# Optimization experiments

Hardware: AMD Instinct MI355X
Metric: run time of the kernel (lower is better)

## Reference

```python
import jax, jax.numpy as jnp
import numpy as np

N, E, D = 50000, 600000, 128
LN_EPS = 1e-5


def setup_inputs() -> dict:
    key = jax.random.key(0)
    ks = jax.random.split(key, 7)
    s = 1.0 / np.sqrt(D)
    x = jax.random.normal(ks[0], (N, D), dtype=jnp.float32)
    edge_index = jax.random.randint(ks[1], (2, E), 0, N, dtype=jnp.int32)
    Wq = jax.random.normal(ks[2], (D, D), dtype=jnp.float32) * s
    Wk = jax.random.normal(ks[3], (D, D), dtype=jnp.float32) * s
    Wv = jax.random.normal(ks[4], (D, D), dtype=jnp.float32) * s
    Wo = jax.random.normal(ks[5], (D, D), dtype=jnp.float32) * s
    bo = jnp.zeros((D,), dtype=jnp.float32)
    gamma = jnp.ones((D,), dtype=jnp.float32)
    beta = jnp.zeros((D,), dtype=jnp.float32)
    return {"x": x, "edge_index": edge_index, "Wq": Wq, "Wk": Wk,
            "Wv": Wv, "Wo": Wo, "bo": bo, "gamma": gamma, "beta": beta}


def reference(x, edge_index, Wq, Wk, Wv, Wo, bo, gamma, beta):
    src, dst = edge_index[0], edge_index[1]
    # gather endpoint features, project (torch Linear: y = x @ W.T)
    q = x[dst] @ Wq.T                      # [E, D]
    k = x[src] @ Wk.T                      # [E, D]
    v = x[src] @ Wv.T                      # [E, D]
    logits = jnp.sum(q * k, axis=-1, keepdims=True) / np.sqrt(D)  # [E, 1]
    msg = jax.nn.sigmoid(logits) * v       # [E, D]
    agg = jax.ops.segment_sum(msg, dst, num_segments=N)  # scatter-add -> [N, D]
    out = agg @ Wo.T + bo
    h = x + out
    # LayerNorm over last dim
    mu = jnp.mean(h, axis=-1, keepdims=True)
    var = jnp.mean(jnp.square(h - mu), axis=-1, keepdims=True)
    return (h - mu) * jax.lax.rsqrt(var + LN_EPS) * gamma + beta
```

## Files before the change

### kernel.cpp

```cpp
#include <hip/hip_runtime.h>
#include <math.h>


#define BM 64
#define QSCALE -0.08838834764831845f

typedef __attribute__((ext_vector_type(8))) short bfrag;
typedef __attribute__((ext_vector_type(4))) float f32x4;

__device__ __forceinline__ short f2bf(float f) {
    union { float f; unsigned u; } v; v.f = f;
    unsigned r = v.u + 0x7FFFu + ((v.u >> 16) & 1u);
    return (short)(r >> 16);
}
__device__ __forceinline__ float bf2f(short h) {
    union { unsigned u; float f; } v;
    v.u = ((unsigned)(unsigned short)h) << 16;
    return v.f;
}
__device__ __forceinline__ float klo(unsigned w) {
    union { unsigned u; float f; } v; v.u = w << 16; return v.f;
}
__device__ __forceinline__ float vhi(unsigned w) {
    union { unsigned u; float f; } v; v.u = w & 0xffff0000u; return v.f;
}

#define SWZ(x, pat) __int_as_float(__builtin_amdgcn_ds_swizzle(__float_as_int(x), pat))

__global__ __launch_bounds__(256) void zero_prep(
    const float* __restrict__ Wq, const float* __restrict__ Wk,
    const float* __restrict__ Wv, const float* __restrict__ Wo,
    short* __restrict__ whi, short* __restrict__ wlo,
    int* __restrict__ hist, int N)
{
    int g = blockIdx.x * 256 + threadIdx.x;
    if (g < N) hist[g] = 0;
    if (g < 65536) {
        const float* Ws[4] = {Wq, Wk, Wv, Wo};
        float f = Ws[g >> 14][g & 16383];
        short h = f2bf(f);
        short l = f2bf(f - bf2f(h));
        whi[g] = h; wlo[g] = l;
    }
}

__global__ __launch_bounds__(256) void qkv_mfma(
    const float* __restrict__ x,
    const short* __restrict__ whi, const short* __restrict__ wlo,
    unsigned short* __restrict__ Q16, unsigned short* __restrict__ KV16, int N)
{
    __shared__ short xs_hi[64][136];
    __shared__ short xs_lo[64][136];

    const int tid = threadIdx.x;
    const int row0 = blockIdx.x * BM;
    const int mat  = blockIdx.y;

    #pragma unroll
    for (int i = 0; i < 8; ++i) {
        int idx = tid + 256 * i;
        int r = idx >> 5;
        int c4 = idx & 31;
        int gr = row0 + r;
        float4 val = make_float4(0.f, 0.f, 0.f, 0.f);
        if (gr < N) val = ((const float4*)(x + (size_t)gr * 128))[c4];
        short4 h, l;
        h.x = f2bf(val.x); l.x = f2bf(val.x - bf2f(h.x));
        h.y = f2bf(val.y); l.y = f2bf(val.y - bf2f(h.y));
        h.z = f2bf(val.z); l.z = f2bf(val.z - bf2f(h.z));
        h.w = f2bf(val.w); l.w = f2bf(val.w - bf2f(h.w));
        *((short4*)&xs_hi[r][c4 * 4]) = h;
        *((short4*)&xs_lo[r][c4 * 4]) = l;
    }
    __syncthreads();

    const int wid  = tid >> 6;
    const int lane = tid & 63;
    const int n16  = lane & 15;
    const int quad = lane >> 4;

    const short* __restrict__ WH = whi + mat * 16384;
    const short* __restrict__ WL = wlo + mat * 16384;
    const f32x4 zero = {0.f, 0.f, 0.f, 0.f};
    f32x4 acc[4][2];
    #pragma unroll
    for (int t = 0; t < 4; ++t) { acc[t][0] = zero; acc[t][1] = zero; }

    #pragma unroll
    for (int kc = 0; kc < 4; ++kc) {
        int k0 = kc * 32 + quad * 8;
        bfrag ah[4], al[4], bh[2], bl[2];
        #pragma unroll
        for (int t = 0; t < 4; ++t) {
            ah[t] = *((const bfrag*)&xs_hi[t * 16 + n16][k0]);
            al[t] = *((const bfrag*)&xs_lo[t * 16 + n16][k0]);
        }
        #pragma unroll
        for (int c = 0; c < 2; ++c) {
            int wr = (wid * 2 + c) * 16 + n16;
            bh[c] = *((const bfrag*)(WH + wr * 128 + k0));
            bl[c] = *((const bfrag*)(WL + wr * 128 + k0));
        }
        #pragma unroll
        for (int t = 0; t < 4; ++t)
            #pragma unroll
            for (int c = 0; c < 2; ++c) {
                acc[t][c] = __builtin_amdgcn_mfma_f32_16x16x32_bf16(ah[t], bh[c], acc[t][c], 0, 0, 0);
                acc[t][c] = __builtin_amdgcn_mfma_f32_16x16x32_bf16(al[t], bh[c], acc[t][c], 0, 0, 0);
                acc[t][c] = __builtin_amdgcn_mfma_f32_16x16x32_bf16(ah[t], bl[c], acc[t][c], 0, 0, 0);
            }
    }

    #pragma unroll
    for (int t = 0; t < 4; ++t)
        #pragma unroll
        for (int r = 0; r < 4; ++r) {
            int grow = row0 + t * 16 + quad * 4 + r;
            if (grow < N) {
                int c0 = (wid * 2 + 0) * 16 + n16;
                int c1 = (wid * 2 + 1) * 16 + n16;
                if (mat == 0) {
                    Q16[(size_t)grow * 128 + c0] = (unsigned short)f2bf(acc[t][0][r] * QSCALE);
                    Q16[(size_t)grow * 128 + c1] = (unsigned short)f2bf(acc[t][1][r] * QSCALE);
                } else {
                    size_t base = (size_t)grow * 256 + (mat - 1);
                    KV16[base + 2 * c0] = (unsigned short)f2bf(acc[t][0][r]);
                    KV16[base + 2 * c1] = (unsigned short)f2bf(acc[t][1][r]);
                }
            }
        }
}

__global__ __launch_bounds__(256) void hist_kernel(
    const int* __restrict__ ei, int* __restrict__ hist, int E)
{
    int e = blockIdx.x * blockDim.x + threadIdx.x;
    if (e < E) atomicAdd(&hist[ei[E + e]], 1);
}

#define SCAN_TPB 256
#define SCAN_EPT 4

__global__ __launch_bounds__(SCAN_TPB) void scan_partial(
    const int* __restrict__ hist, int* __restrict__ offs,
    int* __restrict__ blockSums, int N)
{
    __shared__ int sdata[SCAN_TPB];
    int b = blockIdx.x;
    int t = threadIdx.x;
    int base = b * SCAN_TPB * SCAN_EPT + t * SCAN_EPT;
    int v[SCAN_EPT];
    int tot = 0;
    #pragma unroll
    for (int j = 0; j < SCAN_EPT; ++j) {
        int idx = base + j;
        v[j] = (idx < N) ? hist[idx] : 0;
        tot += v[j];
    }
    sdata[t] = tot;
    __syncthreads();
    for (int off = 1; off < SCAN_TPB; off <<= 1) {
        int xv = (t >= off) ? sdata[t - off] : 0;
        __syncthreads();
        sdata[t] += xv;
        __syncthreads();
    }
    int run = sdata[t] - tot;
    #pragma unroll
    for (int j = 0; j < SCAN_EPT; ++j) {
        int idx = base + j;
        if (idx < N) offs[idx] = run;
        run += v[j];
    }
    if (t == SCAN_TPB - 1) blockSums[b] = sdata[t];
}

__global__ __launch_bounds__(256) void scan_add(
    int* __restrict__ offs, int* __restrict__ starts,
    const int* __restrict__ blockSums, int N, int nb)
{
    __shared__ int bs[64];
    int t = threadIdx.x;
    if (t < 64) {
        int v = (t < nb) ? blockSums[t] : 0;
        #pragma unroll
        for (int off = 1; off < 64; off <<= 1) {
            int u = __shfl_up(v, off);
            if (t >= off) v += u;
        }
        bs[t] = v;
    }
    __syncthreads();
    int idx = blockIdx.x * blockDim.x + threadIdx.x;
    if (idx < N) {
        int blk = idx >> 10;
        int pref = (blk == 0) ? 0 : bs[blk - 1];
        int vv = offs[idx] + pref;
        offs[idx] = vv;
        starts[idx] = vv;
    }
}

__global__ __launch_bounds__(256) void scatter_kernel(
    const int* __restrict__ ei, int* __restrict__ offs,
    int* __restrict__ ssrc, int E)
{
    int e = blockIdx.x * blockDim.x + threadIdx.x;
    if (e < E) {
        int d = ei[E + e];
        int pos = atomicAdd(&offs[d], 1);
        ssrc[pos] = ei[e];
    }
}

__global__ __launch_bounds__(256) void node_agg(
    const int* __restrict__ ssrc,
    const int* __restrict__ starts,
    const int* __restrict__ endoffs,
    const unsigned short* __restrict__ Q16,
    const unsigned short* __restrict__ KV16,
    float* __restrict__ agg, int N)
{
    int node = blockIdx.x * 4 + (threadIdx.x >> 6);
    if (node >= N) return;
    int lane = threadIdx.x & 63;
    int eg   = lane >> 4;
    int sl   = lane & 15;
    int start = starts[node];
    int end   = endoffs[node];

    if (start >= end) {
        if (eg == 0) {
            *((float4*)(agg + (size_t)node * 128 + sl * 8))     = make_float4(0.f, 0.f, 0.f, 0.f);
            *((float4*)(agg + (size_t)node * 128 + sl * 8 + 4)) = make_float4(0.f, 0.f, 0.f, 0.f);
        }
        return;
    }

    bfrag qv = *((const bfrag*)(Q16 + (size_t)node * 128 + sl * 8));
    float q0x = bf2f(qv[0]), q0y = bf2f(qv[1]), q0z = bf2f(qv[2]), q0w = bf2f(qv[3]);
    float q1x = bf2f(qv[4]), q1y = bf2f(qv[5]), q1z = bf2f(qv[6]), q1w = bf2f(qv[7]);

    float a0 = 0.f, a1 = 0.f, a2 = 0.f, a3 = 0.f;
    float a4 = 0.f, a5 = 0.f, a6 = 0.f, a7 = 0.f;

    const unsigned short* kvbase = KV16 + sl * 16;

    for (int base = start; base < end; base += 64) {
        int li = base + lane;
        li = (li < end) ? li : (end - 1);
        int sidx = ssrc[li];
        int nb   = end - base;
        if (nb > 64) nb = 64;
        int nbat = (nb + 7) >> 3;

        int s0 = __shfl(sidx, eg);
        int s1 = __shfl(sidx, 4 + eg);
        const unsigned short* kp0 = kvbase + ((size_t)s0 << 8);
        const unsigned short* kp1 = kvbase + ((size_t)s1 << 8);
        uint4 wa0 = *((const uint4*)kp0);
        uint4 wa1 = *((const uint4*)(kp0 + 8));
        uint4 wb0 = *((const uint4*)kp1);
        uint4 wb1 = *((const uint4*)(kp1 + 8));

        for (int b = 0;;) {
            bool more = (b + 1) < nbat;
            uint4 na0, na1, nb0, nb1;
            if (more) {
                int t0 = __shfl(sidx, 8 * (b + 1) + eg);
                int t1 = __shfl(sidx, 8 * (b + 1) + 4 + eg);
                const unsigned short* np0 = kvbase + ((size_t)t0 << 8);
                const unsigned short* np1 = kvbase + ((size_t)t1 << 8);
                na0 = *((const uint4*)np0);
                na1 = *((const uint4*)(np0 + 8));
                nb0 = *((const uint4*)np1);
                nb1 = *((const uint4*)(np1 + 8));
            }

            int ok0 = ((base + 8 * b + eg) < end);
            int ok1 = ((base + 8 * b + 4 + eg) < end);

            float p0, p1;
            p0 = q0x * klo(wa0.x);
            p0 = fmaf(q0y, klo(wa0.y), p0);
            p0 = fmaf(q0z, klo(wa0.z), p0);
            p0 = fmaf(q0w, klo(wa0.w), p0);
            p0 = fmaf(q1x, klo(wa1.x), p0);
            p0 = fmaf(q1y, klo(wa1.y), p0);
            p0 = fmaf(q1z, klo(wa1.z), p0);
            p0 = fmaf(q1w, klo(wa1.w), p0);
            p1 = q0x * klo(wb0.x);
            p1 = fmaf(q0y, klo(wb0.y), p1);
            p1 = fmaf(q0z, klo(wb0.z), p1);
            p1 = fmaf(q0w, klo(wb0.w), p1);
            p1 = fmaf(q1x, klo(wb1.x), p1);
            p1 = fmaf(q1y, klo(wb1.y), p1);
            p1 = fmaf(q1z, klo(wb1.z), p1);
            p1 = fmaf(q1w, klo(wb1.w), p1);

            p0 += SWZ(p0, 0x041F); p1 += SWZ(p1, 0x041F);
            p0 += SWZ(p0, 0x081F); p1 += SWZ(p1, 0x081F);
            p0 += SWZ(p0, 0x101F); p1 += SWZ(p1, 0x101F);
            p0 += SWZ(p0, 0x201F); p1 += SWZ(p1, 0x201F);

            float c0 = __builtin_amdgcn_rcpf(1.f + __expf(p0));
            float c1 = __builtin_amdgcn_rcpf(1.f + __expf(p1));
            if (!ok0) c0 = 0.f;
            if (!ok1) c1 = 0.f;

            a0 = fmaf(c0, vhi(wa0.x), a0); a0 = fmaf(c1, vhi(wb0.x), a0);
            a1 = fmaf(c0, vhi(wa0.y), a1); a1 = fmaf(c1, vhi(wb0.y), a1);
            a2 = fmaf(c0, vhi(wa0.z), a2); a2 = fmaf(c1, vhi(wb0.z), a2);
            a3 = fmaf(c0, vhi(wa0.w), a3); a3 = fmaf(c1, vhi(wb0.w), a3);
            a4 = fmaf(c0, vhi(wa1.x), a4); a4 = fmaf(c1, vhi(wb1.x), a4);
            a5 = fmaf(c0, vhi(wa1.y), a5); a5 = fmaf(c1, vhi(wb1.y), a5);
            a6 = fmaf(c0, vhi(wa1.z), a6); a6 = fmaf(c1, vhi(wb1.z), a6);
            a7 = fmaf(c0, vhi(wa1.w), a7); a7 = fmaf(c1, vhi(wb1.w), a7);

            if (!more) break;
            wa0 = na0; wa1 = na1; wb0 = nb0; wb1 = nb1;
            ++b;
        }
    }

    a0 += SWZ(a0, 0x401F); a1 += SWZ(a1, 0x401F);
    a2 += SWZ(a2, 0x401F); a3 += SWZ(a3, 0x401F);
    a4 += SWZ(a4, 0x401F); a5 += SWZ(a5, 0x401F);
    a6 += SWZ(a6, 0x401F); a7 += SWZ(a7, 0x401F);
    a0 += __shfl_xor(a0, 32); a1 += __shfl_xor(a1, 32);
    a2 += __shfl_xor(a2, 32); a3 += __shfl_xor(a3, 32);
    a4 += __shfl_xor(a4, 32); a5 += __shfl_xor(a5, 32);
    a6 += __shfl_xor(a6, 32); a7 += __shfl_xor(a7, 32);

    if (eg == 0) {
        *((float4*)(agg + (size_t)node * 128 + sl * 8))     = make_float4(a0, a1, a2, a3);
        *((float4*)(agg + (size_t)node * 128 + sl * 8 + 4)) = make_float4(a4, a5, a6, a7);
    }
}

__global__ __launch_bounds__(256) void out_ln_mfma(
    const float* __restrict__ agg,
    const short* __restrict__ whi, const short* __restrict__ wlo,
    const float* __restrict__ bo, const float* __restrict__ x,
    const float* __restrict__ gamma, const float* __restrict__ beta,
    float* __restrict__ out, int N)
{
    __shared__ __align__(16) char smem[64 * 136 * 2 * 2];
    short (*xs_hi)[136] = (short(*)[136])smem;
    short (*xs_lo)[136] = (short(*)[136])(smem + 64 * 136 * 2);
    float (*hs)[132]    = (float(*)[132])smem;

    const int tid = threadIdx.x;
    const int row0 = blockIdx.x * BM;

    #pragma unroll
    for (int i = 0; i < 8; ++i) {
        int idx = tid + 256 * i;
        int r = idx >> 5;
        int c4 = idx & 31;
        int gr = row0 + r;
        float4 val = make_float4(0.f, 0.f, 0.f, 0.f);
        if (gr < N) val = ((const float4*)(agg + (size_t)gr * 128))[c4];
        short4 h, l;
        h.x = f2bf(val.x); l.x = f2bf(val.x - bf2f(h.x));
        h.y = f2bf(val.y); l.y = f2bf(val.y - bf2f(h.y));
        h.z = f2bf(val.z); l.z = f2bf(val.z - bf2f(h.z));
        h.w = f2bf(val.w); l.w = f2bf(val.w - bf2f(h.w));
        *((short4*)&xs_hi[r][c4 * 4]) = h;
        *((short4*)&xs_lo[r][c4 * 4]) = l;
    }
    __syncthreads();

    const int wid  = tid >> 6;
    const int lane = tid & 63;
    const int n16  = lane & 15;
    const int quad = lane >> 4;
    const short* __restrict__ WH = whi + 3 * 16384;
    const short* __restrict__ WL = wlo + 3 * 16384;

    const f32x4 zero = {0.f, 0.f, 0.f, 0.f};
    f32x4 acc[4][2];
    #pragma unroll
    for (int t = 0; t < 4; ++t) { acc[t][0] = zero; acc[t][1] = zero; }

    #pragma unroll
    for (int kc = 0; kc < 4; ++kc) {
        int k0 = kc * 32 + quad * 8;
        bfrag ah[4], al[4], bh[2], bl[2];
        #pragma unroll
        for (int t = 0; t < 4; ++t) {
            ah[t] = *((const bfrag*)&xs_hi[t * 16 + n16][k0]);
            al[t] = *((const bfrag*)&xs_lo[t * 16 + n16][k0]);
        }
        #pragma unroll
        for (int c = 0; c < 2; ++c) {
            int wr = (wid * 2 + c) * 16 + n16;
            bh[c] = *((const bfrag*)(WH + wr * 128 + k0));
            bl[c] = *((const bfrag*)(WL + wr * 128 + k0));
        }
        #pragma unroll
        for (int t = 0; t < 4; ++t)
            #pragma unroll
            for (int c = 0; c < 2; ++c) {
                acc[t][c] = __builtin_amdgcn_mfma_f32_16x16x32_bf16(ah[t], bh[c], acc[t][c], 0, 0, 0);
                acc[t][c] = __builtin_amdgcn_mfma_f32_16x16x32_bf16(al[t], bh[c], acc[t][c], 0, 0, 0);
                acc[t][c] = __builtin_amdgcn_mfma_f32_16x16x32_bf16(ah[t], bl[c], acc[t][c], 0, 0, 0);
            }
    }
    __syncthreads();

    #pragma unroll
    for (int t = 0; t < 4; ++t)
        #pragma unroll
        for (int r = 0; r < 4; ++r) {
            hs[t * 16 + quad * 4 + r][(wid * 2 + 0) * 16 + n16] = acc[t][0][r];
            hs[t * 16 + quad * 4 + r][(wid * 2 + 1) * 16 + n16] = acc[t][1][r];
        }
    __syncthreads();

    {
        int r = tid >> 2;
        int qd = tid & 3;
        int gr = row0 + r;
        float sum = 0.f, sq = 0.f;
        #pragma unroll
        for (int c = 0; c < 32; c += 4) {
            float4 g4 = *((float4*)&hs[r][qd * 32 + c]);
            float4 b4 = *((const float4*)(bo + qd * 32 + c));
            float4 x4 = make_float4(0.f, 0.f, 0.f, 0.f);
            if (gr < N) x4 = *((const float4*)(x + (size_t)gr * 128 + qd * 32 + c));
            float4 h = make_float4(g4.x + b4.x + x4.x, g4.y + b4.y + x4.y,
                                   g4.z + b4.z + x4.z, g4.w + b4.w + x4.w);
            *((float4*)&hs[r][qd * 32 + c]) = h;
            sum += h.x + h.y + h.z + h.w;
            sq += h.x * h.x + h.y * h.y + h.z * h.z + h.w * h.w;
        }
        sum += __shfl_xor(sum, 1); sum += __shfl_xor(sum, 2);
        sq  += __shfl_xor(sq, 1);  sq  += __shfl_xor(sq, 2);
        float mu = sum * (1.f / 128.f);
        float var = sq * (1.f / 128.f) - mu * mu;
        float rs = rsqrtf(var + 1e-5f);
        if (gr < N) {
            #pragma unroll
            for (int c = 0; c < 32; c += 4) {
                float4 h = *((float4*)&hs[r][qd * 32 + c]);
                float4 g = *((const float4*)(gamma + qd * 32 + c));
                float4 b = *((const float4*)(beta + qd * 32 + c));
                float4 o = make_float4((h.x - mu) * rs * g.x + b.x,
                                       (h.y - mu) * rs * g.y + b.y,
                                       (h.z - mu) * rs * g.z + b.z,
                                       (h.w - mu) * rs * g.w + b.w);
                *((float4*)(out + (size_t)gr * 128 + qd * 32 + c)) = o;
            }
        }
    }
}

extern "C" void kernel_launch(void* const* d_in, const int* in_sizes, int n_in,
                              void* d_out, int out_size, void* d_ws, size_t ws_size,
                              hipStream_t stream) {
    const float* x     = (const float*)d_in[0];
    const int*   ei    = (const int*)d_in[1];
    const float* Wq    = (const float*)d_in[2];
    const float* Wk    = (const float*)d_in[3];
    const float* Wv    = (const float*)d_in[4];
    const float* Wo    = (const float*)d_in[5];
    const float* bo    = (const float*)d_in[6];
    const float* gamma = (const float*)d_in[7];
    const float* beta  = (const float*)d_in[8];
    const int N = in_sizes[0] / 128;
    const int E = in_sizes[1] / 2;
    const size_t ND = (size_t)N * 128;

    unsigned short* Q16  = (unsigned short*)d_ws;
    unsigned short* KV16 = Q16 + ND;
    float* agg = (float*)(KV16 + 2 * ND);
    int* hist      = (int*)(agg + ND);
    int* offs      = hist + N;
    int* starts    = offs + N;
    int* blockSums = starts + N;
    int* ssrc      = blockSums + 256;
    short* whi     = (short*)(ssrc + E);
    short* wlo     = whi + 4 * 16384;

    const int gzp = ((N > 65536 ? N : 65536) + 255) / 256;
    zero_prep<<<gzp, 256, 0, stream>>>(Wq, Wk, Wv, Wo, whi, wlo, hist, N);

    hist_kernel<<<(E + 255) / 256, 256, 0, stream>>>(ei, hist, E);
    const int nScanBlocks = (N + SCAN_TPB * SCAN_EPT - 1) / (SCAN_TPB * SCAN_EPT);
    scan_partial<<<nScanBlocks, SCAN_TPB, 0, stream>>>(hist, offs, blockSums, N);
    scan_add<<<(N + 255) / 256, 256, 0, stream>>>(offs, starts, blockSums, N, nScanBlocks);
    scatter_kernel<<<(E + 255) / 256, 256, 0, stream>>>(ei, offs, ssrc, E);

    const int gq = (N + BM - 1) / BM;
    qkv_mfma<<<dim3(gq, 3), 256, 0, stream>>>(x, whi, wlo, Q16, KV16, N);

    node_agg<<<(N + 3) / 4, 256, 0, stream>>>(ssrc, starts, offs, Q16, KV16, agg, N);

    out_ln_mfma<<<gq, 256, 0, stream>>>(agg, whi, wlo, bo, x, gamma, beta,
                                        (float*)d_out, N);
}
```

Before: 276.0 us.

## Compute Q/K/V in one block per row tile with register-resident x fragments

The QKV projection no longer launches a separate grid slice per weight matrix. Each block now loads and splits its 64 rows of x into bf16 hi/lo once, holding them directly in MFMA A-fragment registers without LDS, and loops over the three matrices. Each wave owns 16 rows and all 128 output columns. This removes the threefold re-read and re-conversion of x and the shared-memory staging and barrier. In exchange it cuts the grid to a third, serialises the three matrices inside a block, and makes each wave fetch the whole weight matrix from global/L2 rather than a slice.

```diff
diff --git a/kernel.cpp b/kernel.cpp
--- a/kernel.cpp
+++ b/kernel.cpp
@@ -49,86 +49,69 @@
     const short* __restrict__ whi, const short* __restrict__ wlo,
     unsigned short* __restrict__ Q16, unsigned short* __restrict__ KV16, int N)
 {
-    __shared__ short xs_hi[64][136];
-    __shared__ short xs_lo[64][136];
-
-    const int tid = threadIdx.x;
-    const int row0 = blockIdx.x * BM;
-    const int mat  = blockIdx.y;
-
-    #pragma unroll
-    for (int i = 0; i < 8; ++i) {
-        int idx = tid + 256 * i;
-        int r = idx >> 5;
-        int c4 = idx & 31;
-        int gr = row0 + r;
-        float4 val = make_float4(0.f, 0.f, 0.f, 0.f);
-        if (gr < N) val = ((const float4*)(x + (size_t)gr * 128))[c4];
-        short4 h, l;
-        h.x = f2bf(val.x); l.x = f2bf(val.x - bf2f(h.x));
-        h.y = f2bf(val.y); l.y = f2bf(val.y - bf2f(h.y));
-        h.z = f2bf(val.z); l.z = f2bf(val.z - bf2f(h.z));
-        h.w = f2bf(val.w); l.w = f2bf(val.w - bf2f(h.w));
-        *((short4*)&xs_hi[r][c4 * 4]) = h;
-        *((short4*)&xs_lo[r][c4 * 4]) = l;
-    }
-    __syncthreads();
-
-    const int wid  = tid >> 6;
+    const int tid  = threadIdx.x;
     const int lane = tid & 63;
     const int n16  = lane & 15;
     const int quad = lane >> 4;
-
-    const short* __restrict__ WH = whi + mat * 16384;
-    const short* __restrict__ WL = wlo + mat * 16384;
-    const f32x4 zero = {0.f, 0.f, 0.f, 0.f};
-    f32x4 acc[4][2];
-    #pragma unroll
-    for (int t = 0; t < 4; ++t) { acc[t][0] = zero; acc[t][1] = zero; }
-
+    const int rowbase = blockIdx.x * BM + (tid >> 6) * 16;
+    const int arow = rowbase + n16;
+    const bool rok = arow < N;
+
+    bfrag ah[4], al[4];
     #pragma unroll
     for (int kc = 0; kc < 4; ++kc) {
-        int k0 = kc * 32 + quad * 8;
-        bfrag ah[4], al[4], bh[2], bl[2];
-        #pragma unroll
-        for (int t = 0; t < 4; ++t) {
-            ah[t] = *((const bfrag*)&xs_hi[t * 16 + n16][k0]);
-            al[t] = *((const bfrag*)&xs_lo[t * 16 + n16][k0]);
-        }
-        #pragma unroll
-        for (int c = 0; c < 2; ++c) {
-            int wr = (wid * 2 + c) * 16 + n16;
-            bh[c] = *((const bfrag*)(WH + wr * 128 + k0));
-            bl[c] = *((const bfrag*)(WL + wr * 128 + k0));
-        }
-        #pragma unroll
-        for (int t = 0; t < 4; ++t)
+        const float* p = x + (size_t)arow * 128 + kc * 32 + quad * 8;
+        float4 f0 = make_float4(0.f, 0.f, 0.f, 0.f);
+        float4 f1 = make_float4(0.f, 0.f, 0.f, 0.f);
+        if (rok) { f0 = *((const float4*)p); f1 = *((const float4*)(p + 4)); }
+        float f[8] = {f0.x, f0.y, f0.z, f0.w, f1.x, f1.y, f1.z, f1.w};
+        #pragma unroll
+        for (int j = 0; j < 8; ++j) {
+            union { float f; unsigned u; } v; v.f = f[j];
+            union { unsigned u; float f; } hv; hv.u = v.u & 0xffff0000u;
+            ah[kc][j] = (short)(v.u >> 16);
+            al[kc][j] = f2bf(f[j] - hv.f);
+        }
+    }
+
+    #pragma unroll 1
+    for (int mat = 0; mat < 3; ++mat) {
+        const short* __restrict__ WH = whi + mat * 16384;
+        const short* __restrict__ WL = wlo + mat * 16384;
+        f32x4 acc[8];
+        #pragma unroll
+        for (int nt = 0; nt < 8; ++nt) acc[nt] = (f32x4){0.f, 0.f, 0.f, 0.f};
+
+        #pragma unroll
+        for (int kc = 0; kc < 4; ++kc) {
+            int k0 = kc * 32 + quad * 8;
             #pragma unroll
-            for (int c = 0; c < 2; ++c) {
-                acc[t][c] = __builtin_amdgcn_mfma_f32_16x16x32_bf16(ah[t], bh[c], acc[t][c], 0, 0, 0);
-                acc[t][c] = __builtin_amdgcn_mfma_f32_16x16x32_bf16(al[t], bh[c], acc[t][c], 0, 0, 0);
-                acc[t][c] = __builtin_amdgcn_mfma_f32_16x16x32_bf16(ah[t], bl[c], acc[t][c], 0, 0, 0);
+            for (int nt = 0; nt < 8; ++nt) {
+                int wr = nt * 16 + n16;
+                bfrag bh = *((const bfrag*)(WH + wr * 128 + k0));
+                bfrag bl = *((const bfrag*)(WL + wr * 128 + k0));
+                acc[nt] = __builtin_amdgcn_mfma_f32_16x16x32_bf16(ah[kc], bh, acc[nt], 0, 0, 0);
+                acc[nt] = __builtin_amdgcn_mfma_f32_16x16x32_bf16(al[kc], bh, acc[nt], 0, 0, 0);
+                acc[nt] = __builtin_amdgcn_mfma_f32_16x16x32_bf16(ah[kc], bl, acc[nt], 0, 0, 0);
             }
-    }
-
-    #pragma unroll
-    for (int t = 0; t < 4; ++t)
-        #pragma unroll
-        for (int r = 0; r < 4; ++r) {
-            int grow = row0 + t * 16 + quad * 4 + r;
-            if (grow < N) {
-                int c0 = (wid * 2 + 0) * 16 + n16;
-                int c1 = (wid * 2 + 1) * 16 + n16;
-                if (mat == 0) {
-                    Q16[(size_t)grow * 128 + c0] = (unsigned short)f2bf(acc[t][0][r] * QSCALE);
-                    Q16[(size_t)grow * 128 + c1] = (unsigned short)f2bf(acc[t][1][r] * QSCALE);
-                } else {
-                    size_t base = (size_t)grow * 256 + (mat - 1);
-                    KV16[base + 2 * c0] = (unsigned short)f2bf(acc[t][0][r]);
-                    KV16[base + 2 * c1] = (unsigned short)f2bf(acc[t][1][r]);
+        }
+
+        #pragma unroll
+        for (int nt = 0; nt < 8; ++nt) {
+            int col = nt * 16 + n16;
+            #pragma unroll
+            for (int r = 0; r < 4; ++r) {
+                int grow = rowbase + quad * 4 + r;
+                if (grow < N) {
+                    if (mat == 0) {
+                        Q16[(size_t)grow * 128 + col] = (unsigned short)f2bf(acc[nt][r] * QSCALE);
+                    } else {
+                        KV16[(size_t)grow * 256 + 2 * col + (mat - 1)] = (unsigned short)f2bf(acc[nt][r]);
+                    }
                 }
             }
         }
+    }
 }
 
 __global__ __launch_bounds__(256) void hist_kernel(
@@ -493,7 +476,7 @@
     scatter_kernel<<<(E + 255) / 256, 256, 0, stream>>>(ei, offs, ssrc, E);
 
     const int gq = (N + BM - 1) / BM;
-    qkv_mfma<<<dim3(gq, 3), 256, 0, stream>>>(x, whi, wlo, Q16, KV16, N);
+    qkv_mfma<<<gq, 256, 0, stream>>>(x, whi, wlo, Q16, KV16, N);
 
     node_agg<<<(N + 3) / 4, 256, 0, stream>>>(ssrc, starts, offs, Q16, KV16, agg, N);
 
```

Measured after the change: 340.8 us. 23.5% more time.

## Fuse CSR preprocessing into one cooperative kernel and loop QKV over matrices

Applied to the files above, without the earlier changes.

Replaces the five preprocessing launches (zero/weight split, histogram, two-stage scan, scatter) with a single cooperative kernel that uses grid-wide syncs between phases, and falls back to the old launches if the cooperative launch fails. The QKV projection now loops over the three weight matrices inside one block, so each x tile is loaded and split into bf16 hi/lo once rather than three times. The goal is less launch overhead and less redundant x traffic. The cost is grid-sync latency, a fixed 1024-block grid that must fit co-resident, and a third as many QKV blocks, which reduces parallelism.

```diff
diff --git a/kernel.cpp b/kernel.cpp
--- a/kernel.cpp
+++ b/kernel.cpp
@@ -1,5 +1,8 @@
 #include <hip/hip_runtime.h>
+#include <hip/hip_cooperative_groups.h>
 #include <math.h>
+
+namespace cg = cooperative_groups;
 
 
 #define BM 64
@@ -26,6 +29,88 @@
 }
 
 #define SWZ(x, pat) __int_as_float(__builtin_amdgcn_ds_swizzle(__float_as_int(x), pat))
+
+__global__ __launch_bounds__(256) void preprocess_coop(
+    const int* __restrict__ ei,
+    const float* __restrict__ Wq, const float* __restrict__ Wk,
+    const float* __restrict__ Wv, const float* __restrict__ Wo,
+    short* __restrict__ whi, short* __restrict__ wlo,
+    int* __restrict__ hist, int* __restrict__ offs, int* __restrict__ starts,
+    int* __restrict__ blockSums, int* __restrict__ ssrc,
+    int N, int E, int nScan)
+{
+    cg::grid_group grid = cg::this_grid();
+    __shared__ int sdata[256];
+    const int t = threadIdx.x;
+    const int gtid = blockIdx.x * 256 + t;
+    const int gsize = gridDim.x * 256;
+
+    for (int i = gtid; i < N; i += gsize) hist[i] = 0;
+    for (int g = gtid; g < 65536; g += gsize) {
+        const float* Ws[4] = {Wq, Wk, Wv, Wo};
+        float f = Ws[g >> 14][g & 16383];
+        short h = f2bf(f);
+        whi[g] = h; wlo[g] = f2bf(f - bf2f(h));
+    }
+    grid.sync();
+
+    for (int e = gtid; e < E; e += gsize) atomicAdd(&hist[ei[E + e]], 1);
+    grid.sync();
+
+    for (int chunk = blockIdx.x; chunk < nScan; chunk += gridDim.x) {
+        int base = chunk * 1024 + t * 4;
+        int v[4]; int tot = 0;
+        #pragma unroll
+        for (int j = 0; j < 4; ++j) {
+            int idx = base + j;
+            v[j] = (idx < N) ? hist[idx] : 0;
+            tot += v[j];
+        }
+        sdata[t] = tot;
+        __syncthreads();
+        for (int off = 1; off < 256; off <<= 1) {
+            int xv = (t >= off) ? sdata[t - off] : 0;
+            __syncthreads();
+            sdata[t] += xv;
+            __syncthreads();
+        }
+        int run = sdata[t] - tot;
+        #pragma unroll
+        for (int j = 0; j < 4; ++j) {
+            int idx = base + j;
+            if (idx < N) offs[idx] = run;
+            run += v[j];
+        }
+        if (t == 255) blockSums[chunk] = sdata[t];
+        __syncthreads();
+    }
+    grid.sync();
+
+    if (blockIdx.x == 0 && t < 64) {
+        int orig = (t < nScan) ? blockSums[t] : 0;
+        int v = orig;
+        #pragma unroll
+        for (int off = 1; off < 64; off <<= 1) {
+            int u = __shfl_up(v, off);
+            if (t >= off) v += u;
+        }
+        if (t < nScan) blockSums[t] = v - orig;
+    }
+    grid.sync();
+
+    for (int i = gtid; i < N; i += gsize) {
+        int vv = offs[i] + blockSums[i >> 10];
+        offs[i] = vv;
+        starts[i] = vv;
+    }
+    grid.sync();
+
+    for (int e = gtid; e < E; e += gsize) {
+        int d = ei[E + e];
+        int pos = atomicAdd(&offs[d], 1);
+        ssrc[pos] = ei[e];
+    }
+}
 
 __global__ __launch_bounds__(256) void zero_prep(
     const float* __restrict__ Wq, const float* __restrict__ Wk,
@@ -44,6 +129,88 @@
     }
 }
 
+__global__ __launch_bounds__(256) void hist_kernel(
+    const int* __restrict__ ei, int* __restrict__ hist, int E)
+{
+    int e = blockIdx.x * blockDim.x + threadIdx.x;
+    if (e < E) atomicAdd(&hist[ei[E + e]], 1);
+}
+
+#define SCAN_TPB 256
+#define SCAN_EPT 4
+
+__global__ __launch_bounds__(SCAN_TPB) void scan_partial(
+    const int* __restrict__ hist, int* __restrict__ offs,
+    int* __restrict__ blockSums, int N)
+{
+    __shared__ int sdata[SCAN_TPB];
+    int b = blockIdx.x;
+    int t = threadIdx.x;
+    int base = b * SCAN_TPB * SCAN_EPT + t * SCAN_EPT;
+    int v[SCAN_EPT];
+    int tot = 0;
+    #pragma unroll
+    for (int j = 0; j < SCAN_EPT; ++j) {
+        int idx = base + j;
+        v[j] = (idx < N) ? hist[idx] : 0;
+        tot += v[j];
+    }
+    sdata[t] = tot;
+    __syncthreads();
+    for (int off = 1; off < SCAN_TPB; off <<= 1) {
+        int xv = (t >= off) ? sdata[t - off] : 0;
+        __syncthreads();
+        sdata[t] += xv;
+        __syncthreads();
+    }
+    int run = sdata[t] - tot;
+    #pragma unroll
+    for (int j = 0; j < SCAN_EPT; ++j) {
+        int idx = base + j;
+        if (idx < N) offs[idx] = run;
+        run += v[j];
+    }
+    if (t == SCAN_TPB - 1) blockSums[b] = sdata[t];
+}
+
+__global__ __launch_bounds__(256) void scan_add(
+    int* __restrict__ offs, int* __restrict__ starts,
+    const int* __restrict__ blockSums, int N, int nb)
+{
+    __shared__ int bs[64];
+    int t = threadIdx.x;
+    if (t < 64) {
+        int v = (t < nb) ? blockSums[t] : 0;
+        #pragma unroll
+        for (int off = 1; off < 64; off <<= 1) {
+            int u = __shfl_up(v, off);
+            if (t >= off) v += u;
+        }
+        bs[t] = v;
+    }
+    __syncthreads();
+    int idx = blockIdx.x * blockDim.x + threadIdx.x;
+    if (idx < N) {
+        int blk = idx >> 10;
+        int pref = (blk == 0) ? 0 : bs[blk - 1];
+        int vv = offs[idx] + pref;
+        offs[idx] = vv;
+        starts[idx] = vv;
+    }
+}
+
+__global__ __launch_bounds__(256) void scatter_kernel(
+    const int* __restrict__ ei, int* __restrict__ offs,
+    int* __restrict__ ssrc, int E)
+{
+    int e = blockIdx.x * blockDim.x + threadIdx.x;
+    if (e < E) {
+        int d = ei[E + e];
+        int pos = atomicAdd(&offs[d], 1);
+        ssrc[pos] = ei[e];
+    }
+}
+
 __global__ __launch_bounds__(256) void qkv_mfma(
     const float* __restrict__ x,
     const short* __restrict__ whi, const short* __restrict__ wlo,
@@ -54,7 +221,6 @@
 
     const int tid = threadIdx.x;
     const int row0 = blockIdx.x * BM;
-    const int mat  = blockIdx.y;
 
     #pragma unroll
     for (int i = 0; i < 8; ++i) {
@@ -79,137 +245,57 @@
     const int n16  = lane & 15;
     const int quad = lane >> 4;
 
-    const short* __restrict__ WH = whi + mat * 16384;
-    const short* __restrict__ WL = wlo + mat * 16384;
-    const f32x4 zero = {0.f, 0.f, 0.f, 0.f};
-    f32x4 acc[4][2];
-    #pragma unroll
-    for (int t = 0; t < 4; ++t) { acc[t][0] = zero; acc[t][1] = zero; }
-
-    #pragma unroll
-    for (int kc = 0; kc < 4; ++kc) {
-        int k0 = kc * 32 + quad * 8;
-        bfrag ah[4], al[4], bh[2], bl[2];
-        #pragma unroll
-        for (int t = 0; t < 4; ++t) {
-            ah[t] = *((const bfrag*)&xs_hi[t * 16 + n16][k0]);
-            al[t] = *((const bfrag*)&xs_lo[t * 16 + n16][k0]);
-        }
-        #pragma unroll
-        for (int c = 0; c < 2; ++c) {
-            int wr = (wid * 2 + c) * 16 + n16;
-            bh[c] = *((const bfrag*)(WH + wr * 128 + k0));
-            bl[c] = *((const bfrag*)(WL + wr * 128 + k0));
+    #pragma unroll 1
+    for (int mat = 0; mat < 3; ++mat) {
+        const short* __restrict__ WH = whi + mat * 16384;
+        const short* __restrict__ WL = wlo + mat * 16384;
+        const f32x4 zero = {0.f, 0.f, 0.f, 0.f};
+        f32x4 acc[4][2];
+        #pragma unroll
+        for (int t = 0; t < 4; ++t) { acc[t][0] = zero; acc[t][1] = zero; }
+
+        #pragma unroll
+        for (int kc = 0; kc < 4; ++kc) {
+            int k0 = kc * 32 + quad * 8;
+            bfrag ah[4], al[4], bh[2], bl[2];
+            #pragma unroll
+            for (int t = 0; t < 4; ++t) {
+                ah[t] = *((const bfrag*)&xs_hi[t * 16 + n16][k0]);
+                al[t] = *((const bfrag*)&xs_lo[t * 16 + n16][k0]);
+            }
+            #pragma unroll
+            for (int c = 0; c < 2; ++c) {
+                int wr = (wid * 2 + c) * 16 + n16;
+                bh[c] = *((const bfrag*)(WH + wr * 128 + k0));
+                bl[c] = *((const bfrag*)(WL + wr * 128 + k0));
+            }
+            #pragma unroll
+            for (int t = 0; t < 4; ++t)
+                #pragma unroll
+                for (int c = 0; c < 2; ++c) {
+                    acc[t][c] = __builtin_amdgcn_mfma_f32_16x16x32_bf16(ah[t], bh[c], acc[t][c], 0, 0, 0);
+                    acc[t][c] = __builtin_amdgcn_mfma_f32_16x16x32_bf16(al[t], bh[c], acc[t][c], 0, 0, 0);
+                    acc[t][c] = __builtin_amdgcn_mfma_f32_16x16x32_bf16(ah[t], bl[c], acc[t][c], 0, 0, 0);
+                }
         }
         #pragma unroll
         for (int t = 0; t < 4; ++t)
             #pragma unroll
-            for (int c = 0; c < 2; ++c) {
-                acc[t][c] = __builtin_amdgcn_mfma_f32_16x16x32_bf16(ah[t], bh[c], acc[t][c], 0, 0, 0);
-                acc[t][c] = __builtin_amdgcn_mfma_f32_16x16x32_bf16(al[t], bh[c], acc[t][c], 0, 0, 0);
-                acc[t][c] = __builtin_amdgcn_mfma_f32_16x16x32_bf16(ah[t], bl[c], acc[t][c], 0, 0, 0);
-            }
-    }
-
-    #pragma unroll
-    for (int t = 0; t < 4; ++t)
-        #pragma unroll
-        for (int r = 0; r < 4; ++r) {
-            int grow = row0 + t * 16 + quad * 4 + r;
-            if (grow < N) {
-                int c0 = (wid * 2 + 0) * 16 + n16;
-                int c1 = (wid * 2 + 1) * 16 + n16;
-                if (mat == 0) {
-                    Q16[(size_t)grow * 128 + c0] = (unsigned short)f2bf(acc[t][0][r] * QSCALE);
-                    Q16[(size_t)grow * 128 + c1] = (unsigned short)f2bf(acc[t][1][r] * QSCALE);
-                } else {
-                    size_t base = (size_t)grow * 256 + (mat - 1);
-                    KV16[base + 2 * c0] = (unsigned short)f2bf(acc[t][0][r]);
-                    KV16[base + 2 * c1] = (unsigned short)f2bf(acc[t][1][r]);
+            for (int r = 0; r < 4; ++r) {
+                int grow = row0 + t * 16 + quad * 4 + r;
+                if (grow < N) {
+                    int c0 = (wid * 2 + 0) * 16 + n16;
+                    int c1 = (wid * 2 + 1) * 16 + n16;
+                    if (mat == 0) {
+                        Q16[(size_t)grow * 128 + c0] = (unsigned short)f2bf(acc[t][0][r] * QSCALE);
+                        Q16[(size_t)grow * 128 + c1] = (unsigned short)f2bf(acc[t][1][r] * QSCALE);
+                    } else {
+                        size_t base = (size_t)grow * 256 + (mat - 1);
+                        KV16[base + 2 * c0] = (unsigned short)f2bf(acc[t][0][r]);
+                        KV16[base + 2 * c1] = (unsigned short)f2bf(acc[t][1][r]);
+                    }
                 }
             }
-        }
-}
-
-__global__ __launch_bounds__(256) void hist_kernel(
-    const int* __restrict__ ei, int* __restrict__ hist, int E)
-{
-    int e = blockIdx.x * blockDim.x + threadIdx.x;
-    if (e < E) atomicAdd(&hist[ei[E + e]], 1);
-}
-
-#define SCAN_TPB 256
-#define SCAN_EPT 4
-
-__global__ __launch_bounds__(SCAN_TPB) void scan_partial(
-    const int* __restrict__ hist, int* __restrict__ offs,
-    int* __restrict__ blockSums, int N)
-{
-    __shared__ int sdata[SCAN_TPB];
-    int b = blockIdx.x;
-    int t = threadIdx.x;
-    int base = b * SCAN_TPB * SCAN_EPT + t * SCAN_EPT;
-    int v[SCAN_EPT];
-    int tot = 0;
-    #pragma unroll
-    for (int j = 0; j < SCAN_EPT; ++j) {
-        int idx = base + j;
-        v[j] = (idx < N) ? hist[idx] : 0;
-        tot += v[j];
-    }
-    sdata[t] = tot;
-    __syncthreads();
-    for (int off = 1; off < SCAN_TPB; off <<= 1) {
-        int xv = (t >= off) ? sdata[t - off] : 0;
-        __syncthreads();
-        sdata[t] += xv;
-        __syncthreads();
-    }
-    int run = sdata[t] - tot;
-    #pragma unroll
-    for (int j = 0; j < SCAN_EPT; ++j) {
-        int idx = base + j;
-        if (idx < N) offs[idx] = run;
-        run += v[j];
-    }
-    if (t == SCAN_TPB - 1) blockSums[b] = sdata[t];
-}
-
-__global__ __launch_bounds__(256) void scan_add(
-    int* __restrict__ offs, int* __restrict__ starts,
-    const int* __restrict__ blockSums, int N, int nb)
-{
-    __shared__ int bs[64];
-    int t = threadIdx.x;
-    if (t < 64) {
-        int v = (t < nb) ? blockSums[t] : 0;
-        #pragma unroll
-        for (int off = 1; off < 64; off <<= 1) {
-            int u = __shfl_up(v, off);
-            if (t >= off) v += u;
-        }
-        bs[t] = v;
-    }
-    __syncthreads();
-    int idx = blockIdx.x * blockDim.x + threadIdx.x;
-    if (idx < N) {
-        int blk = idx >> 10;
-        int pref = (blk == 0) ? 0 : bs[blk - 1];
-        int vv = offs[idx] + pref;
-        offs[idx] = vv;
-        starts[idx] = vv;
-    }
-}
-
-__global__ __launch_bounds__(256) void scatter_kernel(
-    const int* __restrict__ ei, int* __restrict__ offs,
-    int* __restrict__ ssrc, int E)
-{
-    int e = blockIdx.x * blockDim.x + threadIdx.x;
-    if (e < E) {
-        int d = ei[E + e];
-        int pos = atomicAdd(&offs[d], 1);
-        ssrc[pos] = ei[e];
     }
 }
 
@@ -483,17 +569,34 @@
     short* whi     = (short*)(ssrc + E);
     short* wlo     = whi + 4 * 16384;
 
-    const int gzp = ((N > 65536 ? N : 65536) + 255) / 256;
-    zero_prep<<<gzp, 256, 0, stream>>>(Wq, Wk, Wv, Wo, whi, wlo, hist, N);
-
-    hist_kernel<<<(E + 255) / 256, 256, 0, stream>>>(ei, hist, E);
-    const int nScanBlocks = (N + SCAN_TPB * SCAN_EPT - 1) / (SCAN_TPB * SCAN_EPT);
-    scan_partial<<<nScanBlocks, SCAN_TPB, 0, stream>>>(hist, offs, blockSums, N);
-    scan_add<<<(N + 255) / 256, 256, 0, stream>>>(offs, starts, blockSums, N, nScanBlocks);
-    scatter_kernel<<<(E + 255) / 256, 256, 0, stream>>>(ei, offs, ssrc, E);
+    const int nScan = (N + 1023) / 1024;
+
+    {
+        const int*   eip = ei;
+        const float *wqp = Wq, *wkp = Wk, *wvp = Wv, *wop = Wo;
+        short *whip = whi, *wlop = wlo;
+        int *histp = hist, *offsp = offs, *startsp = starts,
+            *bsp = blockSums, *ssrcp = ssrc;
+        int Nv = N, Ev = E, nsv = nScan;
+        void* cargs[] = {
+            (void*)&eip, (void*)&wqp, (void*)&wkp, (void*)&wvp, (void*)&wop,
+            (void*)&whip, (void*)&wlop, (void*)&histp, (void*)&offsp,
+            (void*)&startsp, (void*)&bsp, (void*)&ssrcp,
+            (void*)&Nv, (void*)&Ev, (void*)&nsv };
+        hipError_t cerr = hipLaunchCooperativeKernel(
+            (void*)preprocess_coop, dim3(1024), dim3(256), cargs, 0, stream);
+        if (cerr != hipSuccess) {
+            const int gzp = ((N > 65536 ? N : 65536) + 255) / 256;
+            zero_prep<<<gzp, 256, 0, stream>>>(Wq, Wk, Wv, Wo, whi, wlo, hist, N);
+            hist_kernel<<<(E + 255) / 256, 256, 0, stream>>>(ei, hist, E);
+            scan_partial<<<nScan, SCAN_TPB, 0, stream>>>(hist, offs, blockSums, N);
+            scan_add<<<(N + 255) / 256, 256, 0, stream>>>(offs, starts, blockSums, N, nScan);
+            scatter_kernel<<<(E + 255) / 256, 256, 0, stream>>>(ei, offs, ssrc, E);
+        }
+    }
 
     const int gq = (N + BM - 1) / BM;
-    qkv_mfma<<<dim3(gq, 3), 256, 0, stream>>>(x, whi, wlo, Q16, KV16, N);
+    qkv_mfma<<<gq, 256, 0, stream>>>(x, whi, wlo, Q16, KV16, N);
 
     node_agg<<<(N + 3) / 4, 256, 0, stream>>>(ssrc, starts, offs, Q16, KV16, agg, N);
 
```

Result: slower. 775.5 us (+181.0%).
